# Kernel tuning notes

Measured on AMD Instinct MI355X. Metric: run time of the kernel, lower is better.

Reference implementation:

```python
import jax, jax.numpy as jnp
import numpy as np
import math

N_EXPERTS = 32
K_SEL = 4
IN_C = 1024
OUT_C = 1024
BATCH = 4096


def setup_inputs() -> dict:
    key = jax.random.key(0)
    kx, ki, kw = jax.random.split(key, 3)
    x = jax.random.normal(kx, (BATCH, IN_C), dtype=jnp.float32)
    idx = jax.random.randint(ki, (BATCH, K_SEL), 0, N_EXPERTS, dtype=jnp.int64)
    # xavier_uniform with gain=sqrt(2) (relu) on (n, in_c, out_c):
    # fan_in = in_c, fan_out = out_c for each expert's 2D slice
    gain = math.sqrt(2.0)
    bound = gain * math.sqrt(6.0 / (IN_C + OUT_C))
    w = jax.random.uniform(kw, (N_EXPERTS, IN_C, OUT_C), dtype=jnp.float32,
                           minval=-bound, maxval=bound)
    b = jnp.zeros((N_EXPERTS, 1, OUT_C), dtype=jnp.float32)
    return {"x": x, "idx": idx, "w": w, "b": b}


def reference(x, idx, w, b):
    # Per-sample selection of k of n FC layers:
    # out[bat, k, o] = relu( x[bat] @ w[idx[bat,k]] + b[idx[bat,k]] )
    # Computed densely over all n experts then gathered, which avoids
    # materializing a (B, K, in_c, out_c) gathered-weight tensor.
    y_all = jnp.einsum('bi,nio->bno', x, w) + b[:, 0, :][None]  # (B, n, out_c)
    out = jnp.take_along_axis(y_all, idx[:, :, None], axis=1)   # (B, K, out_c)
    return jax.nn.relu(out)
```

## Files before the change

kernel.cpp:

```cpp
#include <hip/hip_runtime.h>
#include <hip/hip_bf16.h>

#define N_EXPERTS 32
#define K_SEL 4
#define IN_C 1024
#define OUT_C 1024
#define BATCH 4096
#define NTOK (BATCH * K_SEL)

#define BM 128
#define BN 128
#define BK 64
#define MAX_TILES (N_EXPERTS + NTOK / BM)

#define XB_ELEMS (BATCH * IN_C)
#define CTRL_OFF_BYTES ((size_t)XB_ELEMS * 2)

#define WS_NTILES 0
#define WS_TABLE 8
#define WS_ROWLIST (WS_TABLE + MAX_TILES * 4)
#define CTRL_INTS (WS_ROWLIST + NTOK)
#define WS_COUNTS (CTRL_INTS)
#define WS_CURSOR (CTRL_INTS + 32)

typedef __attribute__((ext_vector_type(4))) float f32x4;
typedef __attribute__((ext_vector_type(8))) short bf16x8;
typedef __attribute__((ext_vector_type(8))) unsigned short u16x8;

__device__ __forceinline__ unsigned short f2bf(float f) {
    union { float f; unsigned u; } v; v.f = f;
    unsigned r = v.u + 0x7fffu + ((v.u >> 16) & 1u);
    return (unsigned short)(r >> 16);
}

__device__ __forceinline__ void gload16(const void* g, void* l) {
    __builtin_amdgcn_global_load_lds(
        (const __attribute__((address_space(1))) unsigned int*)g,
        (__attribute__((address_space(3))) unsigned int*)l, 16, 0, 0);
}


#define XCONV_B0 1
#define XCONV_NB (XB_ELEMS / 2048)
#define PREP_NWG (XCONV_B0 + XCONV_NB)

__global__ __launch_bounds__(256)
void prep_kernel(const float* __restrict__ x, const int* __restrict__ idx,
                 unsigned short* __restrict__ xb, int* __restrict__ ctrl) {
    const int bid = blockIdx.x;
    const int t = threadIdx.x;

    if (bid >= XCONV_B0) {
        int i = ((bid - XCONV_B0) * 256 + t) << 3;
        f32x4 v0 = *(const f32x4*)(x + i);
        f32x4 v1 = *(const f32x4*)(x + i + 4);
        u16x8 o;
        o[0] = f2bf(v0[0]); o[1] = f2bf(v0[1]); o[2] = f2bf(v0[2]); o[3] = f2bf(v0[3]);
        o[4] = f2bf(v1[0]); o[5] = f2bf(v1[1]); o[6] = f2bf(v1[2]); o[7] = f2bf(v1[3]);
        *(u16x8*)(xb + i) = o;
    } else {
        __shared__ int cnt[N_EXPERTS], base[N_EXPERTS], tbase[N_EXPERTS];
        if (t < N_EXPERTS) cnt[t] = 0;
        __syncthreads();
        #pragma unroll 4
        for (int i = 0; i < NTOK / 256; ++i) {
            int e = idx[i * 256 + t] & (N_EXPERTS - 1);
            atomicAdd(&cnt[e], 1);
        }
        __syncthreads();
        if (t == 0) {
            int off = 0, tiles = 0;
            for (int e = 0; e < N_EXPERTS; ++e) {
                base[e] = off;
                tbase[e] = tiles;
                int c = cnt[e];
                tiles += (c + BM - 1) / BM;
                off += c;
            }
            ctrl[WS_NTILES] = tiles;
        }
        __syncthreads();
        if (t < N_EXPERTS) {
            int c = cnt[t], off = base[t], tt = tbase[t];
            for (int u = 0; u < c; u += BM, ++tt) {
                ctrl[WS_TABLE + tt * 4 + 0] = t;
                ctrl[WS_TABLE + tt * 4 + 1] = off + u;
                ctrl[WS_TABLE + tt * 4 + 2] = (c - u) < BM ? (c - u) : BM;
            }
            cnt[t] = off;
        }
        __syncthreads();
        #pragma unroll 4
        for (int i = 0; i < NTOK / 256; ++i) {
            int s = i * 256 + t;
            int e = idx[s] & (N_EXPERTS - 1);
            int p = atomicAdd(&cnt[e], 1);
            ctrl[WS_ROWLIST + p] = s;
        }
    }
}


__global__ __launch_bounds__(256, 3)
void gemm_kernel(const unsigned short* __restrict__ xb,
                 const float* __restrict__ w,
                 const float* __restrict__ bias,
                 const int* __restrict__ ctrl,
                 float* __restrict__ out) {
    const int swz = ((int)blockIdx.x & 7) * ((MAX_TILES * 8) >> 3) + ((int)blockIdx.x >> 3);
    const int tileIdx = swz >> 3;
    const int ntiles = ctrl[WS_NTILES];
    if (tileIdx >= ntiles) return;
    const int e     = ctrl[WS_TABLE + tileIdx * 4 + 0];
    const int list0 = ctrl[WS_TABLE + tileIdx * 4 + 1];
    const int nrows = ctrl[WS_TABLE + tileIdx * 4 + 2];
    const int n0 = (swz & 7) * BN;

    __shared__ unsigned short As[BM][BK];
    __shared__ unsigned short Bs[BN][BK];
    __shared__ int rowtok[BM];

    const int t = threadIdx.x;
    const int lane = t & 63, wv = t >> 6;

    if (t < BM) {
        int r = t < nrows ? t : nrows - 1;
        rowtok[t] = ctrl[WS_ROWLIST + list0 + r];
    }
    __syncthreads();

    const int cg = (lane & 7) ^ (lane >> 3);
    const unsigned short* asrc[4];
    #pragma unroll
    for (int i = 0; i < 4; ++i) {
        int row = (wv << 5) + (i << 3) + (lane >> 3);
        asrc[i] = xb + (size_t)(rowtok[row] >> 2) * IN_C + (cg << 3);
    }

    const int q = t & 31, o = t >> 5;
    const float* bbase = w + ((size_t)e << 20) + (size_t)(o << 3 << 10) + n0 + (q << 2);

    const int wr = (t >> 7) & 1;
    const int wc = (t >> 6) & 1;
    const int lrow = lane & 15, lq = lane >> 4;
    const int afo0 = ((lq) ^ (lrow & 7)) << 4;
    const int afo1 = ((4 + lq) ^ (lrow & 7)) << 4;
    const char* aB = (const char*)&As[wr * 64 + lrow][0];
    const char* bB = (const char*)&Bs[wc * 64 + lrow][0];
    int bfo[2][4];
    #pragma unroll
    for (int kk = 0; kk < 2; ++kk)
        #pragma unroll
        for (int nf = 0; nf < 4; ++nf)
            bfo[kk][nf] = ((((kk << 2) + lq) ^ (lrow & 7) ^ ((2 * nf + (lrow >> 3)) & 7)) << 4);

    f32x4 acc[4][4];
    #pragma unroll
    for (int m = 0; m < 4; ++m)
        #pragma unroll
        for (int n = 0; n < 4; ++n) acc[m][n] = (f32x4)0.f;

    for (int k0 = 0; k0 < IN_C; k0 += BK) {
        __syncthreads();
        f32x4 breg[8];
        const float* bsrc = bbase + ((size_t)k0 << 10);
        #pragma unroll
        for (int r = 0; r < 8; ++r)
            breg[r] = *(const f32x4*)(bsrc + ((size_t)r << 10));
        #pragma unroll
        for (int i = 0; i < 4; ++i)
            gload16(asrc[i] + k0, &As[(wv << 5) + (i << 3)][0]);
        #pragma unroll
        for (int j = 0; j < 4; ++j) {
            const int n = (q << 2) + j;
            const int phys = o ^ (n & 7) ^ ((n >> 3) & 7);
            u16x8 ov;
            #pragma unroll
            for (int r = 0; r < 8; ++r) ov[r] = f2bf(breg[r][j]);
            *(u16x8*)&Bs[n][phys << 3] = ov;
        }
        __syncthreads();

        #pragma unroll
        for (int kk = 0; kk < 2; ++kk) {
            const int afo = kk ? afo1 : afo0;
            bf16x8 a[4], b[4];
            #pragma unroll
            for (int m = 0; m < 4; ++m) a[m] = *(const bf16x8*)(aB + m * 2048 + afo);
            #pragma unroll
            for (int n = 0; n < 4; ++n) b[n] = *(const bf16x8*)(bB + n * 2048 + bfo[kk][n]);
            #pragma unroll
            for (int m = 0; m < 4; ++m)
                #pragma unroll
                for (int n = 0; n < 4; ++n)
                    acc[m][n] = __builtin_amdgcn_mfma_f32_16x16x32_bf16(a[m], b[n], acc[m][n], 0, 0, 0);
        }
    }

    #pragma unroll
    for (int m = 0; m < 4; ++m) {
        #pragma unroll
        for (int j = 0; j < 4; ++j) {
            int row = wr * 64 + m * 16 + lq * 4 + j;
            if (row < nrows) {
                int s = rowtok[row];
                float* orow = out + (size_t)s * OUT_C;
                #pragma unroll
                for (int n = 0; n < 4; ++n) {
                    int col = n0 + wc * 64 + n * 16 + lrow;
                    float vv = acc[m][n][j] + bias[e * OUT_C + col];
                    orow[col] = vv > 0.f ? vv : 0.f;
                }
            }
        }
    }
}


__global__ void count_kernel(const int* __restrict__ idx, int* __restrict__ ctrl) {
    int s = blockIdx.x * blockDim.x + threadIdx.x;
    if (s < NTOK) atomicAdd(&ctrl[WS_COUNTS + (idx[s] & (N_EXPERTS - 1))], 1);
}

__global__ void scan_kernel(int* __restrict__ ctrl) {
    if (threadIdx.x != 0) return;
    int off = 0, tiles = 0;
    for (int e = 0; e < N_EXPERTS; ++e) {
        int c = ctrl[WS_COUNTS + e];
        ctrl[WS_CURSOR + e] = off;
        for (int t = 0; t < c; t += BM) {
            ctrl[WS_TABLE + tiles * 4 + 0] = e;
            ctrl[WS_TABLE + tiles * 4 + 1] = off + t;
            ctrl[WS_TABLE + tiles * 4 + 2] = (c - t) < BM ? (c - t) : BM;
            ++tiles;
        }
        off += c;
    }
    ctrl[WS_NTILES] = tiles;
}

__global__ void scatter_kernel(const int* __restrict__ idx, int* __restrict__ ctrl) {
    int s = blockIdx.x * blockDim.x + threadIdx.x;
    if (s < NTOK) {
        int e = idx[s] & (N_EXPERTS - 1);
        int p = atomicAdd(&ctrl[WS_CURSOR + e], 1);
        ctrl[WS_ROWLIST + p] = s;
    }
}

__global__ __launch_bounds__(256, 2)
void gemm_f32_kernel(const float* __restrict__ x, const float* __restrict__ w,
                     const float* __restrict__ bias, const int* __restrict__ ctrl,
                     float* __restrict__ out) {
    int ntiles = ctrl[WS_NTILES];
    if ((int)blockIdx.x >= ntiles) return;
    const int e     = ctrl[WS_TABLE + blockIdx.x * 4 + 0];
    const int list0 = ctrl[WS_TABLE + blockIdx.x * 4 + 1];
    const int nrows = ctrl[WS_TABLE + blockIdx.x * 4 + 2];
    const int n0 = blockIdx.y * BN;

    __shared__ unsigned short As2[BM][40];
    __shared__ unsigned short Bs2[BN][40];
    __shared__ int rowtok[BM];

    const int t = threadIdx.x;
    if (t < BM) {
        int r = t < nrows ? t : nrows - 1;
        rowtok[t] = ctrl[WS_ROWLIST + list0 + r];
    }
    __syncthreads();

    const int arow = t >> 1, acol0 = (t & 1) * 16;
    const int brow = t >> 3, bcol0 = (t & 7) * 16;
    const float* xbase = x + (size_t)(rowtok[arow] >> 2) * IN_C + acol0;
    const float* wbase = w + (size_t)e * IN_C * OUT_C + (size_t)brow * OUT_C + n0 + bcol0;

    const int lane = t & 63, wid = t >> 6;
    const int wr = wid >> 1, wc = wid & 1;
    const int lrow = lane & 15, lq = lane >> 4;

    f32x4 acc[4][4];
    #pragma unroll
    for (int m = 0; m < 4; ++m)
        #pragma unroll
        for (int n = 0; n < 4; ++n) acc[m][n] = (f32x4)0.f;

    for (int k0 = 0; k0 < IN_C; k0 += 32) {
        __syncthreads();
        #pragma unroll
        for (int u = 0; u < 4; ++u) {
            f32x4 v = *(const f32x4*)(xbase + k0 + 4 * u);
            ushort4 pk;
            pk.x = f2bf(v[0]); pk.y = f2bf(v[1]); pk.z = f2bf(v[2]); pk.w = f2bf(v[3]);
            *(ushort4*)&As2[arow][acol0 + 4 * u] = pk;
        }
        #pragma unroll
        for (int u = 0; u < 4; ++u) {
            f32x4 v = *(const f32x4*)(wbase + (size_t)k0 * OUT_C + 4 * u);
            Bs2[bcol0 + 4 * u + 0][brow] = f2bf(v[0]);
            Bs2[bcol0 + 4 * u + 1][brow] = f2bf(v[1]);
            Bs2[bcol0 + 4 * u + 2][brow] = f2bf(v[2]);
            Bs2[bcol0 + 4 * u + 3][brow] = f2bf(v[3]);
        }
        __syncthreads();

        bf16x8 a[4], b[4];
        #pragma unroll
        for (int m = 0; m < 4; ++m) a[m] = *(const bf16x8*)&As2[wr * 64 + m * 16 + lrow][lq * 8];
        #pragma unroll
        for (int n = 0; n < 4; ++n) b[n] = *(const bf16x8*)&Bs2[wc * 64 + n * 16 + lrow][lq * 8];
        #pragma unroll
        for (int m = 0; m < 4; ++m)
            #pragma unroll
            for (int n = 0; n < 4; ++n)
                acc[m][n] = __builtin_amdgcn_mfma_f32_16x16x32_bf16(a[m], b[n], acc[m][n], 0, 0, 0);
    }

    #pragma unroll
    for (int m = 0; m < 4; ++m) {
        #pragma unroll
        for (int j = 0; j < 4; ++j) {
            int row = wr * 64 + m * 16 + lq * 4 + j;
            if (row < nrows) {
                int s = rowtok[row];
                float* orow = out + (size_t)s * OUT_C;
                #pragma unroll
                for (int n = 0; n < 4; ++n) {
                    int col = n0 + wc * 64 + n * 16 + lrow;
                    float vv = acc[m][n][j] + bias[e * OUT_C + col];
                    orow[col] = vv > 0.f ? vv : 0.f;
                }
            }
        }
    }
}


extern "C" void kernel_launch(void* const* d_in, const int* in_sizes, int n_in,
                              void* d_out, int out_size, void* d_ws, size_t ws_size,
                              hipStream_t stream) {
    const float* x    = (const float*)d_in[0];
    const int*   idx  = (const int*)d_in[1];
    const float* w    = (const float*)d_in[2];
    const float* bias = (const float*)d_in[3];
    float* out = (float*)d_out;

    const size_t need = CTRL_OFF_BYTES + (size_t)(CTRL_INTS + 64) * sizeof(int);
    if (ws_size >= need) {
        unsigned short* xb = (unsigned short*)d_ws;
        int* ctrl = (int*)((char*)d_ws + CTRL_OFF_BYTES);

        prep_kernel<<<PREP_NWG, 256, 0, stream>>>(x, idx, xb, ctrl);
        gemm_kernel<<<MAX_TILES * 8, 256, 0, stream>>>(xb, w, bias, ctrl, out);
    } else {
        int* ctrl = (int*)d_ws;
        hipMemsetAsync(ctrl, 0, (CTRL_INTS + 64) * sizeof(int), stream);
        count_kernel<<<NTOK / 256, 256, 0, stream>>>(idx, ctrl);
        scan_kernel<<<1, 64, 0, stream>>>(ctrl);
        scatter_kernel<<<NTOK / 256, 256, 0, stream>>>(idx, ctrl);
        dim3 grid(MAX_TILES, OUT_C / BN);
        gemm_f32_kernel<<<grid, 256, 0, stream>>>(x, w, bias, ctrl, out);
    }
}
```

Before: 105.3 us.

## Warp-specialize GEMM into producer and consumer waves with double-buffered LDS

Expands the gemm block to 512 threads. Four producer waves load A via direct-to-LDS, prefetch the next W tile into registers, convert it to bf16 and write it into one of two LDS buffers. Four consumer waves run the MFMA loop on the other buffer, with hand-placed waitcnt and s_barrier synchronisation between the two groups. The aim is to overlap the global weight loads and fp32-to-bf16 conversion with matrix math, at the cost of twice the LDS, more waves per block, and fragile manual barrier counting.

```diff
diff --git a/kernel.cpp b/kernel.cpp
--- a/kernel.cpp
+++ b/kernel.cpp
@@ -11,6 +11,7 @@
 #define BM 128
 #define BN 128
 #define BK 64
+#define NKT (IN_C / BK)
 #define MAX_TILES (N_EXPERTS + NTOK / BM)
 
 #define XB_ELEMS (BATCH * IN_C)
@@ -101,7 +102,7 @@
 }
 
 
-__global__ __launch_bounds__(256, 3)
+__global__ __launch_bounds__(512, 3)
 void gemm_kernel(const unsigned short* __restrict__ xb,
                  const float* __restrict__ w,
                  const float* __restrict__ bias,
@@ -116,12 +117,12 @@
     const int nrows = ctrl[WS_TABLE + tileIdx * 4 + 2];
     const int n0 = (swz & 7) * BN;
 
-    __shared__ unsigned short As[BM][BK];
-    __shared__ unsigned short Bs[BN][BK];
+    __shared__ unsigned short As[2][BM][BK];
+    __shared__ unsigned short Bs[2][BN][BK];
     __shared__ int rowtok[BM];
 
     const int t = threadIdx.x;
-    const int lane = t & 63, wv = t >> 6;
+    const int lane = t & 63;
 
     if (t < BM) {
         int r = t < nrows ? t : nrows - 1;
@@ -129,30 +130,192 @@
     }
     __syncthreads();
 
-    const int cg = (lane & 7) ^ (lane >> 3);
-    const unsigned short* asrc[4];
-    #pragma unroll
-    for (int i = 0; i < 4; ++i) {
-        int row = (wv << 5) + (i << 3) + (lane >> 3);
-        asrc[i] = xb + (size_t)(rowtok[row] >> 2) * IN_C + (cg << 3);
-    }
-
-    const int q = t & 31, o = t >> 5;
-    const float* bbase = w + ((size_t)e << 20) + (size_t)(o << 3 << 10) + n0 + (q << 2);
-
-    const int wr = (t >> 7) & 1;
-    const int wc = (t >> 6) & 1;
+    if (t >= 256) {
+        const int p = t & 255;
+        const int pw = p >> 6;
+        const int cg = (lane & 7) ^ (lane >> 3);
+        const unsigned short* asrc[4];
+        #pragma unroll
+        for (int i = 0; i < 4; ++i) {
+            int row = (pw << 5) + (i << 3) + (lane >> 3);
+            asrc[i] = xb + (size_t)(rowtok[row] >> 2) * IN_C + (cg << 3);
+        }
+        const int q = p & 31, o = p >> 5;
+        const float* bbase = w + ((size_t)e << 20) + ((size_t)(o << 3) << 10) + n0 + (q << 2);
+
+        f32x4 brgA[8], brgB[8];
+        #pragma unroll
+        for (int r = 0; r < 8; ++r)
+            brgA[r] = *(const f32x4*)(bbase + ((size_t)r << 10));
+
+#define PRODUCE(J, S, CUR, NXT) {                                              \
+        const int kof = (J) << 6;                                              \
+        _Pragma("unroll")                                                      \
+        for (int i = 0; i < 4; ++i)                                            \
+            gload16(asrc[i] + kof, &As[S][(pw << 5) + (i << 3)][0]);           \
+        __builtin_amdgcn_sched_barrier(0);                                     \
+        if ((J) + 1 < NKT) {                                                   \
+            const float* bs2 = bbase + ((size_t)(((J) + 1) << 6) << 10);       \
+            _Pragma("unroll")                                                  \
+            for (int r = 0; r < 8; ++r)                                        \
+                NXT[r] = *(const f32x4*)(bs2 + ((size_t)r << 10));             \
+        }                                                                      \
+        __builtin_amdgcn_sched_barrier(0);                                     \
+        _Pragma("unroll")                                                      \
+        for (int j = 0; j < 4; ++j) {                                          \
+            const int n = (q << 2) + j;                                        \
+            const int phys = o ^ (n & 7) ^ ((n >> 3) & 7);                     \
+            u16x8 ov;                                                          \
+            _Pragma("unroll")                                                  \
+            for (int r = 0; r < 8; ++r) ov[r] = f2bf(CUR[r][j]);               \
+            *(u16x8*)&Bs[S][n][phys << 3] = ov;                                \
+        }                                                                      \
+        __builtin_amdgcn_sched_barrier(0);                                     \
+        if ((J) + 1 < NKT) asm volatile("s_waitcnt vmcnt(8)" ::: "memory");    \
+        else               asm volatile("s_waitcnt vmcnt(0)" ::: "memory");    \
+        asm volatile("s_waitcnt lgkmcnt(0)" ::: "memory");                     \
+        __builtin_amdgcn_sched_barrier(0);                                     \
+        __builtin_amdgcn_s_barrier();                                          \
+        __builtin_amdgcn_sched_barrier(0); }
+
+        for (int jj = 0; jj < NKT; jj += 2) {
+            PRODUCE(jj,     0, brgA, brgB);
+            PRODUCE(jj + 1, 1, brgB, brgA);
+        }
+    } else {
+        const int wr = (t >> 7) & 1;
+        const int wc = (t >> 6) & 1;
+        const int lrow = lane & 15, lq = lane >> 4;
+        const int afo0 = ((lq) ^ (lrow & 7)) << 4;
+        const int afo1 = ((4 + lq) ^ (lrow & 7)) << 4;
+        const char* aB0 = (const char*)&As[0][wr * 64 + lrow][0];
+        const char* aB1 = (const char*)&As[1][wr * 64 + lrow][0];
+        const char* bB0 = (const char*)&Bs[0][wc * 64 + lrow][0];
+        const char* bB1 = (const char*)&Bs[1][wc * 64 + lrow][0];
+        int bfo[2][4];
+        #pragma unroll
+        for (int kk = 0; kk < 2; ++kk)
+            #pragma unroll
+            for (int nf = 0; nf < 4; ++nf)
+                bfo[kk][nf] = ((((kk << 2) + lq) ^ (lrow & 7) ^ ((2 * nf + (lrow >> 3)) & 7)) << 4);
+
+        f32x4 acc[4][4];
+        #pragma unroll
+        for (int m = 0; m < 4; ++m)
+            #pragma unroll
+            for (int n = 0; n < 4; ++n) acc[m][n] = (f32x4)0.f;
+
+#define CONSUME(AB, BB) {                                                      \
+        _Pragma("unroll")                                                      \
+        for (int kk = 0; kk < 2; ++kk) {                                       \
+            const int afo = kk ? afo1 : afo0;                                  \
+            bf16x8 a[4], b[4];                                                 \
+            _Pragma("unroll")                                                  \
+            for (int m = 0; m < 4; ++m) a[m] = *(const bf16x8*)(AB + m * 2048 + afo); \
+            _Pragma("unroll")                                                  \
+            for (int n = 0; n < 4; ++n) b[n] = *(const bf16x8*)(BB + n * 2048 + bfo[kk][n]); \
+            _Pragma("unroll")                                                  \
+            for (int m = 0; m < 4; ++m)                                        \
+                _Pragma("unroll")                                              \
+                for (int n = 0; n < 4; ++n)                                    \
+                    acc[m][n] = __builtin_amdgcn_mfma_f32_16x16x32_bf16(a[m], b[n], acc[m][n], 0, 0, 0); \
+        } }
+
+#define CBARRIER() { asm volatile("s_waitcnt lgkmcnt(0)" ::: "memory");        \
+                     __builtin_amdgcn_sched_barrier(0);                        \
+                     __builtin_amdgcn_s_barrier();                             \
+                     __builtin_amdgcn_sched_barrier(0); }
+
+        CBARRIER();
+        for (int jj = 0; jj < NKT; jj += 2) {
+            CONSUME(aB0, bB0);
+            CBARRIER();
+            CONSUME(aB1, bB1);
+            if (jj + 2 < NKT) CBARRIER();
+        }
+
+        #pragma unroll
+        for (int m = 0; m < 4; ++m) {
+            #pragma unroll
+            for (int j = 0; j < 4; ++j) {
+                int row = wr * 64 + m * 16 + lq * 4 + j;
+                if (row < nrows) {
+                    int s = rowtok[row];
+                    float* orow = out + (size_t)s * OUT_C;
+                    #pragma unroll
+                    for (int n = 0; n < 4; ++n) {
+                        int col = n0 + wc * 64 + n * 16 + lrow;
+                        float vv = acc[m][n][j] + bias[e * OUT_C + col];
+                        orow[col] = vv > 0.f ? vv : 0.f;
+                    }
+                }
+            }
+        }
+    }
+}
+
+
+__global__ void count_kernel(const int* __restrict__ idx, int* __restrict__ ctrl) {
+    int s = blockIdx.x * blockDim.x + threadIdx.x;
+    if (s < NTOK) atomicAdd(&ctrl[WS_COUNTS + (idx[s] & (N_EXPERTS - 1))], 1);
+}
+
+__global__ void scan_kernel(int* __restrict__ ctrl) {
+    if (threadIdx.x != 0) return;
+    int off = 0, tiles = 0;
+    for (int e = 0; e < N_EXPERTS; ++e) {
+        int c = ctrl[WS_COUNTS + e];
+        ctrl[WS_CURSOR + e] = off;
+        for (int t = 0; t < c; t += BM) {
+            ctrl[WS_TABLE + tiles * 4 + 0] = e;
+            ctrl[WS_TABLE + tiles * 4 + 1] = off + t;
+            ctrl[WS_TABLE + tiles * 4 + 2] = (c - t) < BM ? (c - t) : BM;
+            ++tiles;
+        }
+        off += c;
+    }
+    ctrl[WS_NTILES] = tiles;
+}
+
+__global__ void scatter_kernel(const int* __restrict__ idx, int* __restrict__ ctrl) {
+    int s = blockIdx.x * blockDim.x + threadIdx.x;
+    if (s < NTOK) {
+        int e = idx[s] & (N_EXPERTS - 1);
+        int p = atomicAdd(&ctrl[WS_CURSOR + e], 1);
+        ctrl[WS_ROWLIST + p] = s;
+    }
+}
+
+__global__ __launch_bounds__(256, 2)
+void gemm_f32_kernel(const float* __restrict__ x, const float* __restrict__ w,
+                     const float* __restrict__ bias, const int* __restrict__ ctrl,
+                     float* __restrict__ out) {
+    int ntiles = ctrl[WS_NTILES];
+    if ((int)blockIdx.x >= ntiles) return;
+    const int e     = ctrl[WS_TABLE + blockIdx.x * 4 + 0];
+    const int list0 = ctrl[WS_TABLE + blockIdx.x * 4 + 1];
+    const int nrows = ctrl[WS_TABLE + blockIdx.x * 4 + 2];
+    const int n0 = blockIdx.y * BN;
+
+    __shared__ unsigned short As2[BM][40];
+    __shared__ unsigned short Bs2[BN][40];
+    __shared__ int rowtok[BM];
+
+    const int t = threadIdx.x;
+    if (t < BM) {
+        int r = t < nrows ? t : nrows - 1;
+        rowtok[t] = ctrl[WS_ROWLIST + list0 + r];
+    }
+    __syncthreads();
+
+    const int arow = t >> 1, acol0 = (t & 1) * 16;
+    const int brow = t >> 3, bcol0 = (t & 7) * 16;
+    const float* xbase = x + (size_t)(rowtok[arow] >> 2) * IN_C + acol0;
+    const float* wbase = w + (size_t)e * IN_C * OUT_C + (size_t)brow * OUT_C + n0 + bcol0;
+
+    const int lane = t & 63, wid = t >> 6;
+    const int wr = wid >> 1, wc = wid & 1;
     const int lrow = lane & 15, lq = lane >> 4;
-    const int afo0 = ((lq) ^ (lrow & 7)) << 4;
-    const int afo1 = ((4 + lq) ^ (lrow & 7)) << 4;
-    const char* aB = (const char*)&As[wr * 64 + lrow][0];
-    const char* bB = (const char*)&Bs[wc * 64 + lrow][0];
-    int bfo[2][4];
-    #pragma unroll
-    for (int kk = 0; kk < 2; ++kk)
-        #pragma unroll
-        for (int nf = 0; nf < 4; ++nf)
-            bfo[kk][nf] = ((((kk << 2) + lq) ^ (lrow & 7) ^ ((2 * nf + (lrow >> 3)) & 7)) << 4);
 
     f32x4 acc[4][4];
     #pragma unroll
@@ -160,41 +323,35 @@
         #pragma unroll
         for (int n = 0; n < 4; ++n) acc[m][n] = (f32x4)0.f;
 
-    for (int k0 = 0; k0 < IN_C; k0 += BK) {
-        __syncthreads();
-        f32x4 breg[8];
-        const float* bsrc = bbase + ((size_t)k0 << 10);
-        #pragma unroll
-        for (int r = 0; r < 8; ++r)
-            breg[r] = *(const f32x4*)(bsrc + ((size_t)r << 10));
-        #pragma unroll
-        for (int i = 0; i < 4; ++i)
-            gload16(asrc[i] + k0, &As[(wv << 5) + (i << 3)][0]);
-        #pragma unroll
-        for (int j = 0; j < 4; ++j) {
-            const int n = (q << 2) + j;
-            const int phys = o ^ (n & 7) ^ ((n >> 3) & 7);
-            u16x8 ov;
+    for (int k0 = 0; k0 < IN_C; k0 += 32) {
+        __syncthreads();
+        #pragma unroll
+        for (int u = 0; u < 4; ++u) {
+            f32x4 v = *(const f32x4*)(xbase + k0 + 4 * u);
+            ushort4 pk;
+            pk.x = f2bf(v[0]); pk.y = f2bf(v[1]); pk.z = f2bf(v[2]); pk.w = f2bf(v[3]);
+            *(ushort4*)&As2[arow][acol0 + 4 * u] = pk;
+        }
+        #pragma unroll
+        for (int u = 0; u < 4; ++u) {
+            f32x4 v = *(const f32x4*)(wbase + (size_t)k0 * OUT_C + 4 * u);
+            Bs2[bcol0 + 4 * u + 0][brow] = f2bf(v[0]);
+            Bs2[bcol0 + 4 * u + 1][brow] = f2bf(v[1]);
+            Bs2[bcol0 + 4 * u + 2][brow] = f2bf(v[2]);
+            Bs2[bcol0 + 4 * u + 3][brow] = f2bf(v[3]);
+        }
+        __syncthreads();
+
+        bf16x8 a[4], b[4];
+        #pragma unroll
+        for (int m = 0; m < 4; ++m) a[m] = *(const bf16x8*)&As2[wr * 64 + m * 16 + lrow][lq * 8];
+        #pragma unroll
+        for (int n = 0; n < 4; ++n) b[n] = *(const bf16x8*)&Bs2[wc * 64 + n * 16 + lrow][lq * 8];
+        #pragma unroll
+        for (int m = 0; m < 4; ++m)
             #pragma unroll
-            for (int r = 0; r < 8; ++r) ov[r] = f2bf(breg[r][j]);
-            *(u16x8*)&Bs[n][phys << 3] = ov;
-        }
-        __syncthreads();
-
-        #pragma unroll
-        for (int kk = 0; kk < 2; ++kk) {
-            const int afo = kk ? afo1 : afo0;
-            bf16x8 a[4], b[4];
-            #pragma unroll
-            for (int m = 0; m < 4; ++m) a[m] = *(const bf16x8*)(aB + m * 2048 + afo);
-            #pragma unroll
-            for (int n = 0; n < 4; ++n) b[n] = *(const bf16x8*)(bB + n * 2048 + bfo[kk][n]);
-            #pragma unroll
-            for (int m = 0; m < 4; ++m)
-                #pragma unroll
-                for (int n = 0; n < 4; ++n)
-                    acc[m][n] = __builtin_amdgcn_mfma_f32_16x16x32_bf16(a[m], b[n], acc[m][n], 0, 0, 0);
-        }
+            for (int n = 0; n < 4; ++n)
+                acc[m][n] = __builtin_amdgcn_mfma_f32_16x16x32_bf16(a[m], b[n], acc[m][n], 0, 0, 0);
     }
 
     #pragma unroll
@@ -217,125 +374,6 @@
 }
 
 
-__global__ void count_kernel(const int* __restrict__ idx, int* __restrict__ ctrl) {
-    int s = blockIdx.x * blockDim.x + threadIdx.x;
-    if (s < NTOK) atomicAdd(&ctrl[WS_COUNTS + (idx[s] & (N_EXPERTS - 1))], 1);
-}
-
-__global__ void scan_kernel(int* __restrict__ ctrl) {
-    if (threadIdx.x != 0) return;
-    int off = 0, tiles = 0;
-    for (int e = 0; e < N_EXPERTS; ++e) {
-        int c = ctrl[WS_COUNTS + e];
-        ctrl[WS_CURSOR + e] = off;
-        for (int t = 0; t < c; t += BM) {
-            ctrl[WS_TABLE + tiles * 4 + 0] = e;
-            ctrl[WS_TABLE + tiles * 4 + 1] = off + t;
-            ctrl[WS_TABLE + tiles * 4 + 2] = (c - t) < BM ? (c - t) : BM;
-            ++tiles;
-        }
-        off += c;
-    }
-    ctrl[WS_NTILES] = tiles;
-}
-
-__global__ void scatter_kernel(const int* __restrict__ idx, int* __restrict__ ctrl) {
-    int s = blockIdx.x * blockDim.x + threadIdx.x;
-    if (s < NTOK) {
-        int e = idx[s] & (N_EXPERTS - 1);
-        int p = atomicAdd(&ctrl[WS_CURSOR + e], 1);
-        ctrl[WS_ROWLIST + p] = s;
-    }
-}
-
-__global__ __launch_bounds__(256, 2)
-void gemm_f32_kernel(const float* __restrict__ x, const float* __restrict__ w,
-                     const float* __restrict__ bias, const int* __restrict__ ctrl,
-                     float* __restrict__ out) {
-    int ntiles = ctrl[WS_NTILES];
-    if ((int)blockIdx.x >= ntiles) return;
-    const int e     = ctrl[WS_TABLE + blockIdx.x * 4 + 0];
-    const int list0 = ctrl[WS_TABLE + blockIdx.x * 4 + 1];
-    const int nrows = ctrl[WS_TABLE + blockIdx.x * 4 + 2];
-    const int n0 = blockIdx.y * BN;
-
-    __shared__ unsigned short As2[BM][40];
-    __shared__ unsigned short Bs2[BN][40];
-    __shared__ int rowtok[BM];
-
-    const int t = threadIdx.x;
-    if (t < BM) {
-        int r = t < nrows ? t : nrows - 1;
-        rowtok[t] = ctrl[WS_ROWLIST + list0 + r];
-    }
-    __syncthreads();
-
-    const int arow = t >> 1, acol0 = (t & 1) * 16;
-    const int brow = t >> 3, bcol0 = (t & 7) * 16;
-    const float* xbase = x + (size_t)(rowtok[arow] >> 2) * IN_C + acol0;
-    const float* wbase = w + (size_t)e * IN_C * OUT_C + (size_t)brow * OUT_C + n0 + bcol0;
-
-    const int lane = t & 63, wid = t >> 6;
-    const int wr = wid >> 1, wc = wid & 1;
-    const int lrow = lane & 15, lq = lane >> 4;
-
-    f32x4 acc[4][4];
-    #pragma unroll
-    for (int m = 0; m < 4; ++m)
-        #pragma unroll
-        for (int n = 0; n < 4; ++n) acc[m][n] = (f32x4)0.f;
-
-    for (int k0 = 0; k0 < IN_C; k0 += 32) {
-        __syncthreads();
-        #pragma unroll
-        for (int u = 0; u < 4; ++u) {
-            f32x4 v = *(const f32x4*)(xbase + k0 + 4 * u);
-            ushort4 pk;
-            pk.x = f2bf(v[0]); pk.y = f2bf(v[1]); pk.z = f2bf(v[2]); pk.w = f2bf(v[3]);
-            *(ushort4*)&As2[arow][acol0 + 4 * u] = pk;
-        }
-        #pragma unroll
-        for (int u = 0; u < 4; ++u) {
-            f32x4 v = *(const f32x4*)(wbase + (size_t)k0 * OUT_C + 4 * u);
-            Bs2[bcol0 + 4 * u + 0][brow] = f2bf(v[0]);
-            Bs2[bcol0 + 4 * u + 1][brow] = f2bf(v[1]);
-            Bs2[bcol0 + 4 * u + 2][brow] = f2bf(v[2]);
-            Bs2[bcol0 + 4 * u + 3][brow] = f2bf(v[3]);
-        }
-        __syncthreads();
-
-        bf16x8 a[4], b[4];
-        #pragma unroll
-        for (int m = 0; m < 4; ++m) a[m] = *(const bf16x8*)&As2[wr * 64 + m * 16 + lrow][lq * 8];
-        #pragma unroll
-        for (int n = 0; n < 4; ++n) b[n] = *(const bf16x8*)&Bs2[wc * 64 + n * 16 + lrow][lq * 8];
-        #pragma unroll
-        for (int m = 0; m < 4; ++m)
-            #pragma unroll
-            for (int n = 0; n < 4; ++n)
-                acc[m][n] = __builtin_amdgcn_mfma_f32_16x16x32_bf16(a[m], b[n], acc[m][n], 0, 0, 0);
-    }
-
-    #pragma unroll
-    for (int m = 0; m < 4; ++m) {
-        #pragma unroll
-        for (int j = 0; j < 4; ++j) {
-            int row = wr * 64 + m * 16 + lq * 4 + j;
-            if (row < nrows) {
-                int s = rowtok[row];
-                float* orow = out + (size_t)s * OUT_C;
-                #pragma unroll
-                for (int n = 0; n < 4; ++n) {
-                    int col = n0 + wc * 64 + n * 16 + lrow;
-                    float vv = acc[m][n][j] + bias[e * OUT_C + col];
-                    orow[col] = vv > 0.f ? vv : 0.f;
-                }
-            }
-        }
-    }
-}
-
-
 extern "C" void kernel_launch(void* const* d_in, const int* in_sizes, int n_in,
                               void* d_out, int out_size, void* d_ws, size_t ws_size,
                               hipStream_t stream) {
@@ -351,7 +389,7 @@
         int* ctrl = (int*)((char*)d_ws + CTRL_OFF_BYTES);
 
         prep_kernel<<<PREP_NWG, 256, 0, stream>>>(x, idx, xb, ctrl);
-        gemm_kernel<<<MAX_TILES * 8, 256, 0, stream>>>(xb, w, bias, ctrl, out);
+        gemm_kernel<<<MAX_TILES * 8, 512, 0, stream>>>(xb, w, bias, ctrl, out);
     } else {
         int* ctrl = (int*)d_ws;
         hipMemsetAsync(ctrl, 0, (CTRL_INTS + 64) * sizeof(int), stream);
```

Measured after the change: 104.8 us. About the same (-0.5%).

## Keep a full expert weight column slab in LDS and loop over all token tiles

Applied to the files above, without the earlier changes.

The GEMM now gives each workgroup one (expert, 64-column) pair. It converts the whole 1024x64 weight slab to bf16 into LDS once, then walks every 128-row token tile of that expert. Before, each tile reloaded and reconverted its own fp32 weights, so this removes repeated weight reads and conversion. The cost is about 136KB of LDS per block, one 512-thread block per CU, only 512 workgroups, and uneven work when expert counts differ.

```diff
diff --git a/kernel.cpp b/kernel.cpp
--- a/kernel.cpp
+++ b/kernel.cpp
@@ -9,13 +9,16 @@
 #define NTOK (BATCH * K_SEL)
 
 #define BM 128
-#define BN 128
-#define BK 64
+#define BN2 64
 #define MAX_TILES (N_EXPERTS + NTOK / BM)
 
 #define XB_ELEMS (BATCH * IN_C)
 #define CTRL_OFF_BYTES ((size_t)XB_ELEMS * 2)
 
+#define MS_EBASE 0
+#define MS_ECNT 32
+#define MS_ROWLIST 64
+#define MS_INTS (MS_ROWLIST + NTOK)
 #define WS_NTILES 0
 #define WS_TABLE 8
 #define WS_ROWLIST (WS_TABLE + MAX_TILES * 4)
@@ -59,7 +62,7 @@
         o[4] = f2bf(v1[0]); o[5] = f2bf(v1[1]); o[6] = f2bf(v1[2]); o[7] = f2bf(v1[3]);
         *(u16x8*)(xb + i) = o;
     } else {
-        __shared__ int cnt[N_EXPERTS], base[N_EXPERTS], tbase[N_EXPERTS];
+        __shared__ int cnt[N_EXPERTS], base[N_EXPERTS];
         if (t < N_EXPERTS) cnt[t] = 0;
         __syncthreads();
         #pragma unroll 4
@@ -69,25 +72,14 @@
         }
         __syncthreads();
         if (t == 0) {
-            int off = 0, tiles = 0;
-            for (int e = 0; e < N_EXPERTS; ++e) {
-                base[e] = off;
-                tbase[e] = tiles;
-                int c = cnt[e];
-                tiles += (c + BM - 1) / BM;
-                off += c;
-            }
-            ctrl[WS_NTILES] = tiles;
+            int off = 0;
+            for (int e = 0; e < N_EXPERTS; ++e) { base[e] = off; off += cnt[e]; }
         }
         __syncthreads();
         if (t < N_EXPERTS) {
-            int c = cnt[t], off = base[t], tt = tbase[t];
-            for (int u = 0; u < c; u += BM, ++tt) {
-                ctrl[WS_TABLE + tt * 4 + 0] = t;
-                ctrl[WS_TABLE + tt * 4 + 1] = off + u;
-                ctrl[WS_TABLE + tt * 4 + 2] = (c - u) < BM ? (c - u) : BM;
-            }
-            cnt[t] = off;
+            ctrl[MS_EBASE + t] = base[t];
+            ctrl[MS_ECNT + t] = cnt[t];
+            cnt[t] = base[t];
         }
         __syncthreads();
         #pragma unroll 4
@@ -95,121 +87,136 @@
             int s = i * 256 + t;
             int e = idx[s] & (N_EXPERTS - 1);
             int p = atomicAdd(&cnt[e], 1);
-            ctrl[WS_ROWLIST + p] = s;
-        }
-    }
-}
-
-
-__global__ __launch_bounds__(256, 3)
+            ctrl[MS_ROWLIST + p] = s;
+        }
+    }
+}
+
+
+#define GEMM_NWG (N_EXPERTS * 16)
+
+__global__ __launch_bounds__(512, 1)
 void gemm_kernel(const unsigned short* __restrict__ xb,
                  const float* __restrict__ w,
                  const float* __restrict__ bias,
                  const int* __restrict__ ctrl,
                  float* __restrict__ out) {
-    const int swz = ((int)blockIdx.x & 7) * ((MAX_TILES * 8) >> 3) + ((int)blockIdx.x >> 3);
-    const int tileIdx = swz >> 3;
-    const int ntiles = ctrl[WS_NTILES];
-    if (tileIdx >= ntiles) return;
-    const int e     = ctrl[WS_TABLE + tileIdx * 4 + 0];
-    const int list0 = ctrl[WS_TABLE + tileIdx * 4 + 1];
-    const int nrows = ctrl[WS_TABLE + tileIdx * 4 + 2];
-    const int n0 = (swz & 7) * BN;
-
-    __shared__ unsigned short As[BM][BK];
-    __shared__ unsigned short Bs[BN][BK];
-    __shared__ int rowtok[BM];
+    const int bid = (int)blockIdx.x;
+    const int swz = (bid & 7) * (GEMM_NWG / 8) + (bid >> 3);
+    const int e  = swz >> 4;
+    const int n0 = (swz & 15) << 6;
+
+    __shared__ unsigned short Bp[64 * 1024];
+    __shared__ unsigned short As[128][64];
 
     const int t = threadIdx.x;
     const int lane = t & 63, wv = t >> 6;
 
-    if (t < BM) {
-        int r = t < nrows ? t : nrows - 1;
-        rowtok[t] = ctrl[WS_ROWLIST + list0 + r];
-    }
-    __syncthreads();
-
-    const int cg = (lane & 7) ^ (lane >> 3);
-    const unsigned short* asrc[4];
-    #pragma unroll
-    for (int i = 0; i < 4; ++i) {
-        int row = (wv << 5) + (i << 3) + (lane >> 3);
-        asrc[i] = xb + (size_t)(rowtok[row] >> 2) * IN_C + (cg << 3);
-    }
-
-    const int q = t & 31, o = t >> 5;
-    const float* bbase = w + ((size_t)e << 20) + (size_t)(o << 3 << 10) + n0 + (q << 2);
-
-    const int wr = (t >> 7) & 1;
-    const int wc = (t >> 6) & 1;
+    {
+        const int q = t & 15, o = t >> 4;
+        const float* wsrc = w + ((size_t)e << 20) + ((size_t)(o << 3) << 10) + n0 + (q << 2);
+        #pragma unroll
+        for (int p = 0; p < 4; ++p) {
+            f32x4 r[8];
+            const float* s_ = wsrc + ((size_t)p << 18);
+            #pragma unroll
+            for (int rr = 0; rr < 8; ++rr) r[rr] = *(const f32x4*)(s_ + ((size_t)rr << 10));
+            const int c = (p << 5) + o, chi = c >> 3, clo = c & 7;
+            #pragma unroll
+            for (int j = 0; j < 4; ++j) {
+                const int n = (q << 2) + j;
+                const int kap = (n & 7) ^ ((n >> 3) & 7);
+                u16x8 ov;
+                #pragma unroll
+                for (int rr = 0; rr < 8; ++rr) ov[rr] = f2bf(r[rr][j]);
+                *(u16x8*)&Bp[(n << 10) + (((chi << 3) | (clo ^ kap)) << 3)] = ov;
+            }
+        }
+    }
+
+    const int ebase = ctrl[MS_EBASE + e];
+    const int ecnt  = ctrl[MS_ECNT + e];
+    const int ntile = (ecnt + 127) >> 7;
+
+    const int wr = wv >> 1, wc = wv & 1;
     const int lrow = lane & 15, lq = lane >> 4;
     const int afo0 = ((lq) ^ (lrow & 7)) << 4;
     const int afo1 = ((4 + lq) ^ (lrow & 7)) << 4;
-    const char* aB = (const char*)&As[wr * 64 + lrow][0];
-    const char* bB = (const char*)&Bs[wc * 64 + lrow][0];
-    int bfo[2][4];
+    const char* aB = (const char*)&As[(wr << 5) + lrow][0];
+    const char* bpB[2];
+    int bxo[2][2];
     #pragma unroll
-    for (int kk = 0; kk < 2; ++kk)
-        #pragma unroll
-        for (int nf = 0; nf < 4; ++nf)
-            bfo[kk][nf] = ((((kk << 2) + lq) ^ (lrow & 7) ^ ((2 * nf + (lrow >> 3)) & 7)) << 4);
-
-    f32x4 acc[4][4];
+    for (int nf = 0; nf < 2; ++nf) {
+        const int n = (wc << 5) + (nf << 4) + lrow;
+        bpB[nf] = (const char*)&Bp[n << 10];
+        #pragma unroll
+        for (int kk = 0; kk < 2; ++kk)
+            bxo[kk][nf] = ((((kk << 2) + lq) ^ (n & 7) ^ ((n >> 3) & 7)) << 4);
+    }
+    float bcol[2];
     #pragma unroll
-    for (int m = 0; m < 4; ++m)
-        #pragma unroll
-        for (int n = 0; n < 4; ++n) acc[m][n] = (f32x4)0.f;
-
-    for (int k0 = 0; k0 < IN_C; k0 += BK) {
-        __syncthreads();
-        f32x4 breg[8];
-        const float* bsrc = bbase + ((size_t)k0 << 10);
-        #pragma unroll
-        for (int r = 0; r < 8; ++r)
-            breg[r] = *(const f32x4*)(bsrc + ((size_t)r << 10));
-        #pragma unroll
-        for (int i = 0; i < 4; ++i)
-            gload16(asrc[i] + k0, &As[(wv << 5) + (i << 3)][0]);
-        #pragma unroll
-        for (int j = 0; j < 4; ++j) {
-            const int n = (q << 2) + j;
-            const int phys = o ^ (n & 7) ^ ((n >> 3) & 7);
-            u16x8 ov;
-            #pragma unroll
-            for (int r = 0; r < 8; ++r) ov[r] = f2bf(breg[r][j]);
-            *(u16x8*)&Bs[n][phys << 3] = ov;
-        }
-        __syncthreads();
-
-        #pragma unroll
-        for (int kk = 0; kk < 2; ++kk) {
-            const int afo = kk ? afo1 : afo0;
-            bf16x8 a[4], b[4];
-            #pragma unroll
-            for (int m = 0; m < 4; ++m) a[m] = *(const bf16x8*)(aB + m * 2048 + afo);
-            #pragma unroll
-            for (int n = 0; n < 4; ++n) b[n] = *(const bf16x8*)(bB + n * 2048 + bfo[kk][n]);
-            #pragma unroll
-            for (int m = 0; m < 4; ++m)
-                #pragma unroll
-                for (int n = 0; n < 4; ++n)
-                    acc[m][n] = __builtin_amdgcn_mfma_f32_16x16x32_bf16(a[m], b[n], acc[m][n], 0, 0, 0);
-        }
-    }
-
-    #pragma unroll
-    for (int m = 0; m < 4; ++m) {
-        #pragma unroll
-        for (int j = 0; j < 4; ++j) {
-            int row = wr * 64 + m * 16 + lq * 4 + j;
-            if (row < nrows) {
-                int s = rowtok[row];
-                float* orow = out + (size_t)s * OUT_C;
-                #pragma unroll
-                for (int n = 0; n < 4; ++n) {
-                    int col = n0 + wc * 64 + n * 16 + lrow;
-                    float vv = acc[m][n][j] + bias[e * OUT_C + col];
-                    orow[col] = vv > 0.f ? vv : 0.f;
+    for (int nf = 0; nf < 2; ++nf)
+        bcol[nf] = bias[(e << 10) + n0 + (wc << 5) + (nf << 4) + lrow];
+
+    const int cg = (lane & 7) ^ (lane >> 3);
+
+    __syncthreads();
+
+    for (int mt = 0; mt < ntile; ++mt) {
+        const int lofs = ebase + (mt << 7);
+        const int rem = ecnt - (mt << 7);
+        const int rcap = rem < 128 ? rem : 128;
+
+        const unsigned short* asrc[2];
+        #pragma unroll
+        for (int i = 0; i < 2; ++i) {
+            int row = (wv << 4) + (i << 3) + (lane >> 3);
+            int rr = row < rcap ? row : rcap - 1;
+            asrc[i] = xb + ((size_t)(ctrl[MS_ROWLIST + lofs + rr] >> 2) << 10) + (cg << 3);
+        }
+
+        f32x4 acc[2][2];
+        #pragma unroll
+        for (int m = 0; m < 2; ++m)
+            #pragma unroll
+            for (int n = 0; n < 2; ++n) acc[m][n] = (f32x4)0.f;
+
+        for (int ks = 0; ks < 16; ++ks) {
+            __syncthreads();
+            gload16(asrc[0] + (ks << 6), &As[(wv << 4) + 0][0]);
+            gload16(asrc[1] + (ks << 6), &As[(wv << 4) + 8][0]);
+            __syncthreads();
+
+            const int kso = ks << 7;
+            #pragma unroll
+            for (int kk = 0; kk < 2; ++kk) {
+                const int afo = kk ? afo1 : afo0;
+                bf16x8 a[2], b[2];
+                #pragma unroll
+                for (int m = 0; m < 2; ++m) a[m] = *(const bf16x8*)(aB + m * 2048 + afo);
+                #pragma unroll
+                for (int nf = 0; nf < 2; ++nf) b[nf] = *(const bf16x8*)(bpB[nf] + kso + bxo[kk][nf]);
+                #pragma unroll
+                for (int m = 0; m < 2; ++m)
+                    #pragma unroll
+                    for (int nf = 0; nf < 2; ++nf)
+                        acc[m][nf] = __builtin_amdgcn_mfma_f32_16x16x32_bf16(a[m], b[nf], acc[m][nf], 0, 0, 0);
+            }
+        }
+
+        #pragma unroll
+        for (int m = 0; m < 2; ++m) {
+            #pragma unroll
+            for (int j = 0; j < 4; ++j) {
+                int row = (wr << 5) + (m << 4) + (lq << 2) + j;
+                if (row < rcap) {
+                    int s = ctrl[MS_ROWLIST + lofs + row];
+                    float* orow = out + ((size_t)s << 10) + n0 + (wc << 5);
+                    #pragma unroll
+                    for (int nf = 0; nf < 2; ++nf) {
+                        float vv = acc[m][nf][j] + bcol[nf];
+                        orow[(nf << 4) + lrow] = vv > 0.f ? vv : 0.f;
+                    }
                 }
             }
         }
@@ -257,10 +264,10 @@
     const int e     = ctrl[WS_TABLE + blockIdx.x * 4 + 0];
     const int list0 = ctrl[WS_TABLE + blockIdx.x * 4 + 1];
     const int nrows = ctrl[WS_TABLE + blockIdx.x * 4 + 2];
-    const int n0 = blockIdx.y * BN;
+    const int n0 = blockIdx.y * 128;
 
     __shared__ unsigned short As2[BM][40];
-    __shared__ unsigned short Bs2[BN][40];
+    __shared__ unsigned short Bs2[128][40];
     __shared__ int rowtok[BM];
 
     const int t = threadIdx.x;
@@ -351,14 +358,14 @@
         int* ctrl = (int*)((char*)d_ws + CTRL_OFF_BYTES);
 
         prep_kernel<<<PREP_NWG, 256, 0, stream>>>(x, idx, xb, ctrl);
-        gemm_kernel<<<MAX_TILES * 8, 256, 0, stream>>>(xb, w, bias, ctrl, out);
+        gemm_kernel<<<GEMM_NWG, 512, 0, stream>>>(xb, w, bias, ctrl, out);
     } else {
         int* ctrl = (int*)d_ws;
         hipMemsetAsync(ctrl, 0, (CTRL_INTS + 64) * sizeof(int), stream);
         count_kernel<<<NTOK / 256, 256, 0, stream>>>(idx, ctrl);
         scan_kernel<<<1, 64, 0, stream>>>(ctrl);
         scatter_kernel<<<NTOK / 256, 256, 0, stream>>>(idx, ctrl);
-        dim3 grid(MAX_TILES, OUT_C / BN);
+        dim3 grid(MAX_TILES, OUT_C / 128);
         gemm_f32_kernel<<<grid, 256, 0, stream>>>(x, w, bias, ctrl, out);
     }
 }
```

Result: slower. 162.7 us (+54.4%).
